# Performance work log

Hardware: AMD Instinct MI355X
Metric: run time of the kernel (lower is better)

Reference implementation:

```python
import jax, jax.numpy as jnp
import numpy as np

N = 12288
BASE_SCALE = 0.001  # initial isotropic scale in __init__


def build_rotation(q):
    # q: [N,4] normalized quaternions (r, x, y, z) -> [N,3,3] rotation matrices
    r, x, y, z = q[:, 0], q[:, 1], q[:, 2], q[:, 3]
    R = jnp.stack([
        jnp.stack([1 - 2 * (y * y + z * z), 2 * (x * y - r * z), 2 * (x * z + r * y)], axis=-1),
        jnp.stack([2 * (x * y + r * z), 1 - 2 * (x * x + z * z), 2 * (y * z - r * x)], axis=-1),
        jnp.stack([2 * (x * z - r * y), 2 * (y * z + r * x), 1 - 2 * (x * x + y * y)], axis=-1),
    ], axis=-2)  # [N,3,3]
    return R


def setup_inputs() -> dict:
    key = jax.random.key(0)
    k1, k2 = jax.random.split(key)
    points = jax.random.normal(k1, (N, 3), dtype=jnp.float32)
    quaternions = jax.random.normal(k2, (N, 4), dtype=jnp.float32)
    return {"points": points, "quaternions": quaternions}


def reference(points, quaternions):
    n = points.shape[0]
    # --- initialize_scale: NxN pairwise distances, top-3 smallest, mean ---
    sq = jnp.sum(points * points, axis=1)  # [N]
    d2 = sq[:, None] + sq[None, :] - 2.0 * (points @ points.T)  # [N,N] squared dists
    idx = jnp.arange(n)
    diag = idx[:, None] == idx[None, :]
    d2 = jnp.where(diag, jnp.inf, jnp.maximum(d2, 0.0))
    dist = jnp.sqrt(d2)
    neg_top3, _ = jax.lax.top_k(-dist, 3)  # 3 smallest distances (negated)
    mean_scale = jnp.maximum(jnp.mean(-neg_top3, axis=1), 1e-5)  # [N]
    scales = BASE_SCALE * mean_scale[:, None] * jnp.ones((n, 3), dtype=points.dtype)  # [N,3]
    # --- get_3d_covariance_matrix ---
    qn = quaternions / jnp.linalg.norm(quaternions, axis=1, keepdims=True)
    Rm = build_rotation(qn)  # [N,3,3]
    M = Rm * scales[:, None, :]  # R @ diag(s), [N,3,3]
    cov = jnp.einsum('nij,nkj->nik', M, M)  # M @ M^T, [N,3,3]
    return cov
```

## Files before the change

### kernel.cpp

```cpp
#include <hip/hip_runtime.h>
#include <math.h>


#define N_PTS 12288
#define CHUNK 512
#define NCH   (N_PTS / CHUNK)
#define CELLJ 32
#define IBLK  256
#define NIB   (N_PTS / IBLK)
#define TSTR  257

typedef _Float16 half8 __attribute__((ext_vector_type(8)));
typedef float    f32x4 __attribute__((ext_vector_type(4)));

__device__ __forceinline__ void ins4(float d, float& a0, float& a1,
                                     float& a2, float& a3) {
    const float n0 = fminf(a0, d);
    const float n1 = __builtin_amdgcn_fmed3f(a0, a1, d);
    const float n2 = __builtin_amdgcn_fmed3f(a1, a2, d);
    const float n3 = __builtin_amdgcn_fmed3f(a2, a3, d);
    a0 = n0; a1 = n1; a2 = n2; a3 = n3;
}

__global__ __launch_bounds__(256) void cellmin_mfma(
    const float* __restrict__ pts, float4* __restrict__ ws4)
{
    __shared__ __align__(16) unsigned char shmem[32 * 64 * 8 * 2];
    _Float16* sB = (_Float16*)shmem;
    float*    sT = (float*)shmem;

    const int t    = threadIdx.x;
    const int iblk = blockIdx.x * IBLK;
    const int g    = blockIdx.y;

    for (int idx = t; idx < CHUNK; idx += 256) {
        const int col = idx & 15, b = idx >> 4;
        const int j = g * CHUNK + col * 32 + b;
        const float x = pts[3 * j + 0], y = pts[3 * j + 1], z = pts[3 * j + 2];
        const _Float16 bhx = (_Float16)x, bhy = (_Float16)y, bhz = (_Float16)z;
        const _Float16 blx = (_Float16)(x - (float)bhx);
        const _Float16 bly = (_Float16)(y - (float)bhy);
        const _Float16 blz = (_Float16)(z - (float)bhz);
        const float q = 0.5f * fmaf(z, z, fmaf(y, y, x * x));
        const _Float16 qh = (_Float16)q;
        const _Float16 ql = (_Float16)(q - (float)qh);
        half8 s0;
        s0[0] = -bhx; s0[1] = -bhy; s0[2] = -bhz;
        s0[3] = -bhx; s0[4] = -bhy; s0[5] = -bhz;
        s0[6] = -blx; s0[7] = -bly;
        half8 s1;
        s1 = (_Float16)0;
        s1[0] = -blz; s1[1] = qh; s1[2] = ql;
        *(half8*)&sB[(b * 64 + col) * 8]      = s0;
        *(half8*)&sB[(b * 64 + 16 + col) * 8] = s1;
    }
    {
        half8 zz = (_Float16)0;
        for (int s = t; s < 32 * 32; s += 256)
            *(half8*)&sB[((s >> 5) * 64 + 32 + (s & 31)) * 8] = zz;
    }

    float qi_t;
    {
        const float x = pts[3 * (iblk + t) + 0];
        const float y = pts[3 * (iblk + t) + 1];
        const float z = pts[3 * (iblk + t) + 2];
        qi_t = 0.5f * fmaf(z, z, fmaf(y, y, x * x));
    }

    const int lane = t & 63;
    const int w    = t >> 6;
    const int m    = lane & 15;
    const int quad = lane >> 4;

    half8 afr[4];
    f32x4 mn[4];
    #pragma unroll
    for (int rr = 0; rr < 4; ++rr) {
        const int i = iblk + (4 * w + rr) * 16 + m;
        const float x = pts[3 * i + 0], y = pts[3 * i + 1], z = pts[3 * i + 2];
        const _Float16 ahx = (_Float16)x, ahy = (_Float16)y, ahz = (_Float16)z;
        const _Float16 alx = (_Float16)(x - (float)ahx);
        const _Float16 aly = (_Float16)(y - (float)ahy);
        const _Float16 alz = (_Float16)(z - (float)ahz);
        half8 a = (_Float16)0;
        if (quad == 0) {
            a[0] = ahx; a[1] = ahy; a[2] = ahz;
            a[3] = alx; a[4] = aly; a[5] = alz;
            a[6] = ahx; a[7] = ahy;
        } else if (quad == 1) {
            a[0] = ahz; a[1] = (_Float16)1.0f; a[2] = (_Float16)1.0f;
        }
        afr[rr] = a;
        mn[rr] = INFINITY;
    }
    __syncthreads();

    const f32x4 zero4 = 0.0f;
    #pragma unroll 4
    for (int b = 0; b < 32; ++b) {
        const half8 bf = *(const half8*)&sB[(b * 64 + lane) * 8];
        #pragma unroll
        for (int rr = 0; rr < 4; ++rr) {
            const f32x4 d = __builtin_amdgcn_mfma_f32_16x16x32_f16(
                afr[rr], bf, zero4, 0, 0, 0);
            mn[rr][0] = fminf(mn[rr][0], d[0]);
            mn[rr][1] = fminf(mn[rr][1], d[1]);
            mn[rr][2] = fminf(mn[rr][2], d[2]);
            mn[rr][3] = fminf(mn[rr][3], d[3]);
        }
    }
    __syncthreads();

    #pragma unroll
    for (int rr = 0; rr < 4; ++rr) {
        const int rowb = (4 * w + rr) * 16 + quad * 4;
        #pragma unroll
        for (int reg = 0; reg < 4; ++reg)
            sT[m * TSTR + rowb + reg] = mn[rr][reg];
    }
    __syncthreads();

    float t0 = INFINITY, t1 = INFINITY, t2 = INFINITY, t3 = INFINITY;
    #pragma unroll
    for (int c = 0; c < 16; ++c) {
        const float v = sT[c * TSTR + t] + qi_t;
        const unsigned cid = (unsigned)(g * 16 + c);
        const float pv = __uint_as_float((__float_as_uint(v) & ~511u) | cid);
        ins4(pv, t0, t1, t2, t3);
    }
    ws4[(size_t)g * N_PTS + (iblk + t)] = make_float4(t0, t1, t2, t3);
}

__global__ __launch_bounds__(64) void knn_finalize(
    const float4* __restrict__ ws4, const float* __restrict__ pts,
    float* __restrict__ out)
{
    __shared__ float sS[8];
    const int lane  = threadIdx.x;
    const int il    = lane & 7;
    const int w     = lane >> 3;
    const int ibase = blockIdx.x * 8;
    const int i     = ibase + il;

    float c0 = INFINITY, c1 = INFINITY, c2 = INFINITY, c3 = INFINITY;
    #pragma unroll
    for (int k = 0; k < 3; ++k) {
        const float4 v = ws4[(size_t)(3 * w + k) * N_PTS + i];
        ins4(v.x, c0, c1, c2, c3);
        ins4(v.y, c0, c1, c2, c3);
        ins4(v.z, c0, c1, c2, c3);
        ins4(v.w, c0, c1, c2, c3);
    }

    #pragma unroll
    for (int mask = 8; mask < 64; mask <<= 1) {
        const float p0 = __shfl_xor(c0, mask);
        const float p1 = __shfl_xor(c1, mask);
        const float p2 = __shfl_xor(c2, mask);
        const float p3 = __shfl_xor(c3, mask);
        ins4(p0, c0, c1, c2, c3);
        ins4(p1, c0, c1, c2, c3);
        ins4(p2, c0, c1, c2, c3);
        ins4(p3, c0, c1, c2, c3);
    }

    const float px = pts[3 * i + 0];
    const float py = pts[3 * i + 1];
    const float pz = pts[3 * i + 2];

    float b0 = INFINITY, b1 = INFINITY, b2 = INFINITY, b3 = INFINITY;
    const unsigned cells[4] = {
        __float_as_uint(c0) & 511u, __float_as_uint(c1) & 511u,
        __float_as_uint(c2) & 511u, __float_as_uint(c3) & 511u };
    #pragma unroll
    for (int q = 0; q < 4; ++q) {
        const int cid = (int)cells[q];
        const int jb  = (cid >> 4) * CHUNK + (cid & 15) * CELLJ + w * 4;
        #pragma unroll
        for (int n = 0; n < 4; ++n) {
            const int j = jb + n;
            const float dx = px - pts[3 * j + 0];
            const float dy = py - pts[3 * j + 1];
            const float dz = pz - pts[3 * j + 2];
            const float d2 = fmaf(dz, dz, fmaf(dy, dy, dx * dx));
            ins4(d2, b0, b1, b2, b3);
        }
    }

    #pragma unroll
    for (int mask = 8; mask < 64; mask <<= 1) {
        const float p0 = __shfl_xor(b0, mask);
        const float p1 = __shfl_xor(b1, mask);
        const float p2 = __shfl_xor(b2, mask);
        const float p3 = __shfl_xor(b3, mask);
        ins4(p0, b0, b1, b2, b3);
        ins4(p1, b0, b1, b2, b3);
        ins4(p2, b0, b1, b2, b3);
        ins4(p3, b0, b1, b2, b3);
    }

    if (w == 0) {
        const float d0 = sqrtf(b1);
        const float d1 = sqrtf(b2);
        const float d2 = sqrtf(b3);
        float mean = fmaxf((d0 + d1 + d2) * (1.0f / 3.0f), 1e-5f);
        const float s = 0.001f * mean;
        sS[il] = s * s;
    }
    __syncthreads();

    for (int k = lane; k < 72; k += 64) {
        const int i2 = k / 9, r = k % 9;
        const float v = (r == 0 || r == 4 || r == 8) ? sS[i2] : 0.0f;
        out[(size_t)(ibase + i2) * 9 + r] = v;
    }
}

extern "C" void kernel_launch(void* const* d_in, const int* in_sizes, int n_in,
                              void* d_out, int out_size, void* d_ws, size_t ws_size,
                              hipStream_t stream) {
    const float* pts = (const float*)d_in[0];
    float4* ws4 = (float4*)d_ws;
    float*  out = (float*)d_out;

    cellmin_mfma<<<dim3(NIB, NCH), dim3(256), 0, stream>>>(pts, ws4);
    knn_finalize<<<dim3(N_PTS / 8), dim3(64), 0, stream>>>(ws4, pts, out);
}
```

Before: 75.19 us.

## Switch cell-min pass to 32x32x16 MFMA with 16-point cells

The MFMA distance pass moves from 16x16x32 to 32x32x16 instructions, so each wave covers 32 columns per instruction, and the number of B iterations drops from 32 to 16. Cells shrink to 16 points, giving 32 cells per chunk. The cell id packed into the low float bits grows to 10 bits, and the finalize kernel rescans fewer candidate points per cell. The dead zero-padding of the B tile is no longer written, and an occupancy hint is added. The trade-offs are 16-wide accumulators with more fminf work per instruction, a longer per-column top-4 merge, and a coarser cell-id encoding that gives up more mantissa bits.

```diff
diff --git a/kernel.cpp b/kernel.cpp
--- a/kernel.cpp
+++ b/kernel.cpp
@@ -5,13 +5,14 @@
 #define N_PTS 12288
 #define CHUNK 512
 #define NCH   (N_PTS / CHUNK)
-#define CELLJ 32
+#define CELLJ 16
 #define IBLK  256
 #define NIB   (N_PTS / IBLK)
 #define TSTR  257
-
-typedef _Float16 half8 __attribute__((ext_vector_type(8)));
-typedef float    f32x4 __attribute__((ext_vector_type(4)));
+#define CMASK 1023u
+
+typedef _Float16 half8  __attribute__((ext_vector_type(8)));
+typedef float    f32x16 __attribute__((ext_vector_type(16)));
 
 __device__ __forceinline__ void ins4(float d, float& a0, float& a1,
                                      float& a2, float& a3) {
@@ -22,10 +23,10 @@
     a0 = n0; a1 = n1; a2 = n2; a3 = n3;
 }
 
-__global__ __launch_bounds__(256) void cellmin_mfma(
+__global__ __launch_bounds__(256, 4) void cellmin_mfma(
     const float* __restrict__ pts, float4* __restrict__ ws4)
 {
-    __shared__ __align__(16) unsigned char shmem[32 * 64 * 8 * 2];
+    __shared__ __align__(16) unsigned char shmem[32 * TSTR * 4];
     _Float16* sB = (_Float16*)shmem;
     float*    sT = (float*)shmem;
 
@@ -34,8 +35,8 @@
     const int g    = blockIdx.y;
 
     for (int idx = t; idx < CHUNK; idx += 256) {
-        const int col = idx & 15, b = idx >> 4;
-        const int j = g * CHUNK + col * 32 + b;
+        const int col = idx & 31, b = idx >> 5;
+        const int j = g * CHUNK + col * CELLJ + b;
         const float x = pts[3 * j + 0], y = pts[3 * j + 1], z = pts[3 * j + 2];
         const _Float16 bhx = (_Float16)x, bhy = (_Float16)y, bhz = (_Float16)z;
         const _Float16 blx = (_Float16)(x - (float)bhx);
@@ -48,16 +49,10 @@
         s0[0] = -bhx; s0[1] = -bhy; s0[2] = -bhz;
         s0[3] = -bhx; s0[4] = -bhy; s0[5] = -bhz;
         s0[6] = -blx; s0[7] = -bly;
-        half8 s1;
-        s1 = (_Float16)0;
+        half8 s1 = (_Float16)0;
         s1[0] = -blz; s1[1] = qh; s1[2] = ql;
         *(half8*)&sB[(b * 64 + col) * 8]      = s0;
-        *(half8*)&sB[(b * 64 + 16 + col) * 8] = s1;
-    }
-    {
-        half8 zz = (_Float16)0;
-        for (int s = t; s < 32 * 32; s += 256)
-            *(half8*)&sB[((s >> 5) * 64 + 32 + (s & 31)) * 8] = zz;
+        *(half8*)&sB[(b * 64 + 32 + col) * 8] = s1;
     }
 
     float qi_t;
@@ -70,63 +65,63 @@
 
     const int lane = t & 63;
     const int w    = t >> 6;
-    const int m    = lane & 15;
-    const int quad = lane >> 4;
-
-    half8 afr[4];
-    f32x4 mn[4];
-    #pragma unroll
-    for (int rr = 0; rr < 4; ++rr) {
-        const int i = iblk + (4 * w + rr) * 16 + m;
+    const int m    = lane & 31;
+    const int h    = lane >> 5;
+
+    half8  afr[2];
+    f32x16 mn[2];
+    #pragma unroll
+    for (int tau = 0; tau < 2; ++tau) {
+        const int i = iblk + (2 * w + tau) * 32 + m;
         const float x = pts[3 * i + 0], y = pts[3 * i + 1], z = pts[3 * i + 2];
         const _Float16 ahx = (_Float16)x, ahy = (_Float16)y, ahz = (_Float16)z;
         const _Float16 alx = (_Float16)(x - (float)ahx);
         const _Float16 aly = (_Float16)(y - (float)ahy);
         const _Float16 alz = (_Float16)(z - (float)ahz);
         half8 a = (_Float16)0;
-        if (quad == 0) {
+        if (h == 0) {
             a[0] = ahx; a[1] = ahy; a[2] = ahz;
             a[3] = alx; a[4] = aly; a[5] = alz;
             a[6] = ahx; a[7] = ahy;
-        } else if (quad == 1) {
+        } else {
             a[0] = ahz; a[1] = (_Float16)1.0f; a[2] = (_Float16)1.0f;
         }
-        afr[rr] = a;
-        mn[rr] = INFINITY;
-    }
-    __syncthreads();
-
-    const f32x4 zero4 = 0.0f;
+        afr[tau] = a;
+        mn[tau] = INFINITY;
+    }
+    __syncthreads();
+
+    const f32x16 zero16 = 0.0f;
     #pragma unroll 4
-    for (int b = 0; b < 32; ++b) {
+    for (int b = 0; b < 16; ++b) {
         const half8 bf = *(const half8*)&sB[(b * 64 + lane) * 8];
         #pragma unroll
-        for (int rr = 0; rr < 4; ++rr) {
-            const f32x4 d = __builtin_amdgcn_mfma_f32_16x16x32_f16(
-                afr[rr], bf, zero4, 0, 0, 0);
-            mn[rr][0] = fminf(mn[rr][0], d[0]);
-            mn[rr][1] = fminf(mn[rr][1], d[1]);
-            mn[rr][2] = fminf(mn[rr][2], d[2]);
-            mn[rr][3] = fminf(mn[rr][3], d[3]);
-        }
-    }
-    __syncthreads();
-
-    #pragma unroll
-    for (int rr = 0; rr < 4; ++rr) {
-        const int rowb = (4 * w + rr) * 16 + quad * 4;
+        for (int tau = 0; tau < 2; ++tau) {
+            const f32x16 d = __builtin_amdgcn_mfma_f32_32x32x16_f16(
+                afr[tau], bf, zero16, 0, 0, 0);
+            #pragma unroll
+            for (int r = 0; r < 16; ++r)
+                mn[tau][r] = fminf(mn[tau][r], d[r]);
+        }
+    }
+    __syncthreads();
+
+    #pragma unroll
+    for (int tau = 0; tau < 2; ++tau) {
         #pragma unroll
-        for (int reg = 0; reg < 4; ++reg)
-            sT[m * TSTR + rowb + reg] = mn[rr][reg];
+        for (int r = 0; r < 16; ++r) {
+            const int row = (r & 3) + 8 * (r >> 2) + 4 * h;
+            sT[m * TSTR + (2 * w + tau) * 32 + row] = mn[tau][r];
+        }
     }
     __syncthreads();
 
     float t0 = INFINITY, t1 = INFINITY, t2 = INFINITY, t3 = INFINITY;
-    #pragma unroll
-    for (int c = 0; c < 16; ++c) {
+    #pragma unroll 8
+    for (int c = 0; c < 32; ++c) {
         const float v = sT[c * TSTR + t] + qi_t;
-        const unsigned cid = (unsigned)(g * 16 + c);
-        const float pv = __uint_as_float((__float_as_uint(v) & ~511u) | cid);
+        const unsigned cid = (unsigned)(g * 32 + c);
+        const float pv = __uint_as_float((__float_as_uint(v) & ~CMASK) | cid);
         ins4(pv, t0, t1, t2, t3);
     }
     ws4[(size_t)g * N_PTS + (iblk + t)] = make_float4(t0, t1, t2, t3);
@@ -171,14 +166,14 @@
 
     float b0 = INFINITY, b1 = INFINITY, b2 = INFINITY, b3 = INFINITY;
     const unsigned cells[4] = {
-        __float_as_uint(c0) & 511u, __float_as_uint(c1) & 511u,
-        __float_as_uint(c2) & 511u, __float_as_uint(c3) & 511u };
+        __float_as_uint(c0) & CMASK, __float_as_uint(c1) & CMASK,
+        __float_as_uint(c2) & CMASK, __float_as_uint(c3) & CMASK };
     #pragma unroll
     for (int q = 0; q < 4; ++q) {
         const int cid = (int)cells[q];
-        const int jb  = (cid >> 4) * CHUNK + (cid & 15) * CELLJ + w * 4;
+        const int jb  = (cid >> 5) * CHUNK + (cid & 31) * CELLJ + w * 2;
         #pragma unroll
-        for (int n = 0; n < 4; ++n) {
+        for (int n = 0; n < 2; ++n) {
             const int j = jb + n;
             const float dx = px - pts[3 * j + 0];
             const float dy = py - pts[3 * j + 1];
```

Result: faster. 71.57 us (-4.8%).
